# Kernel tuning notes

Measured on AMD Instinct MI355X. Metric: run time of the kernel, lower is better.

The kernel has to match this reference:

```python
import jax, jax.numpy as jnp
import numpy as np

D_MODEL = 512
NUM_HEADS = 8
D_K = D_MODEL // NUM_HEADS
D_FF = 4 * D_MODEL
EPS = 1e-5


def _pos_encoding(seq_len, d_model, dtype=jnp.float32):
    pos = jnp.arange(seq_len, dtype=jnp.float32)[:, None]              # [S,1]
    div = jnp.exp(jnp.arange(0, d_model, 2, dtype=jnp.float32) * (-np.log(10000.0) / d_model))  # [D/2]
    ang = pos * div                                                      # [S,D/2]
    pe = jnp.stack([jnp.sin(ang), jnp.cos(ang)], axis=-1).reshape(seq_len, d_model)
    return pe.astype(dtype)


def _layernorm(x, g, b):
    mu = jnp.mean(x, axis=-1, keepdims=True)
    var = jnp.mean(jnp.square(x - mu), axis=-1, keepdims=True)
    return (x - mu) * jax.lax.rsqrt(var + EPS) * g + b


def setup_inputs() -> dict:
    key = jax.random.key(0)
    ks = jax.random.split(key, 12)
    B, S, D = 4, 2048, D_MODEL
    s = 1.0 / np.sqrt(D)
    inp = {
        "x": jax.random.normal(ks[0], (B, S, D), jnp.float32),
        "Wq": jax.random.normal(ks[1], (D, D), jnp.float32) * s,
        "bq": jnp.zeros((D,), jnp.float32),
        "Wk": jax.random.normal(ks[2], (D, D), jnp.float32) * s,
        "bk": jnp.zeros((D,), jnp.float32),
        "Wv": jax.random.normal(ks[3], (D, D), jnp.float32) * s,
        "bv": jnp.zeros((D,), jnp.float32),
        "Wo": jax.random.normal(ks[4], (D, D), jnp.float32) * s,
        "bo": jnp.zeros((D,), jnp.float32),
        "g1": jnp.ones((D,), jnp.float32),
        "b1": jnp.zeros((D,), jnp.float32),
        "W_ff1": jax.random.normal(ks[5], (D, D_FF), jnp.float32) * s,
        "b_ff1": jnp.zeros((D_FF,), jnp.float32),
        "W_ff2": jax.random.normal(ks[6], (D_FF, D), jnp.float32) * (1.0 / np.sqrt(D_FF)),
        "b_ff2": jnp.zeros((D,), jnp.float32),
        "g2": jnp.ones((D,), jnp.float32),
        "b2": jnp.zeros((D,), jnp.float32),
    }
    return inp


def reference(x, Wq, bq, Wk, bk, Wv, bv, Wo, bo, g1, b1, W_ff1, b_ff1, W_ff2, b_ff2, g2, b2):
    B, S, D = x.shape
    H, dk = NUM_HEADS, D_K
    # positional encoding (deterministic buffer)
    x = x + _pos_encoding(S, D, x.dtype)[None]
    # projections -> [B,H,S,dk]
    q = (x @ Wq + bq).reshape(B, S, H, dk).transpose(0, 2, 1, 3)
    k = (x @ Wk + bk).reshape(B, S, H, dk).transpose(0, 2, 1, 3)
    v = (x @ Wv + bv).reshape(B, S, H, dk).transpose(0, 2, 1, 3)
    # naive attention: materialized [B,H,S,S] scores (as in original)
    scores = jnp.einsum('bhqd,bhkd->bhqk', q, k) / np.sqrt(dk)
    attn = jax.nn.softmax(scores, axis=-1)
    ctx = jnp.einsum('bhqk,bhkd->bhqd', attn, v)
    ctx = ctx.transpose(0, 2, 1, 3).reshape(B, S, D)
    attn_out = ctx @ Wo + bo
    # residual + LN + FFN + residual + LN
    h = _layernorm(x + attn_out, g1, b1)
    ff = jax.nn.relu(h @ W_ff1 + b_ff1) @ W_ff2 + b_ff2
    return _layernorm(h + ff, g2, b2)
```

## Files before the change

kernel.cpp:

```cpp
#include <hip/hip_runtime.h>

typedef unsigned short u16;
typedef unsigned int u32;
typedef __attribute__((ext_vector_type(8))) short s16x8;
typedef __attribute__((ext_vector_type(2))) float f32x2;
typedef __attribute__((ext_vector_type(4))) float f32x4;
typedef __attribute__((ext_vector_type(16))) float f32x16;
typedef __attribute__((ext_vector_type(2))) u32 u32x2;
typedef __attribute__((ext_vector_type(4))) u32 u32x4;

#define MB (1ull << 20)
#define K1SCALE 0.18033688f

__device__ __forceinline__ u16 f2bf(float f) {
  u32 u = __float_as_uint(f);
  u32 r = (u + 0x7fffu + ((u >> 16) & 1u)) >> 16;
  return (u16)r;
}

__device__ __forceinline__ float bf2f(u16 x) { return __uint_as_float(((u32)x) << 16); }

__device__ __forceinline__ u32 cvtpk(float lo, float hi) {
  u32 r;
  asm("v_cvt_pk_bf16_f32 %0, %1, %2" : "=v"(r) : "v"(lo), "v"(hi));
  return r;
}

__device__ __forceinline__ float max3f(float a, float b, float c) {
  float d;
  asm("v_max3_f32 %0, %1, %2, %3" : "=v"(d) : "v"(a), "v"(b), "v"(c));
  return d;
}

__device__ __forceinline__ f32x2 pk_mul(f32x2 a, f32x2 b) {
  f32x2 d;
  asm("v_pk_mul_f32 %0, %1, %2" : "=v"(d) : "v"(a), "v"(b));
  return d;
}
__device__ __forceinline__ f32x2 pk_add(f32x2 a, f32x2 b) {
  f32x2 d;
  asm("v_pk_add_f32 %0, %1, %2" : "=v"(d) : "v"(a), "v"(b));
  return d;
}

__device__ __forceinline__ void gload16(const u16* g, u16* l) {
  __builtin_amdgcn_global_load_lds((const __attribute__((address_space(1))) void*)g,
                                   (__attribute__((address_space(3))) void*)l, 16, 0, 0);
}

__global__ __launch_bounds__(256) void k_posenc(const float* __restrict__ x,
                                                float* __restrict__ xf, u16* __restrict__ xb) {
  int idx = blockIdx.x * 256 + threadIdx.x;
  int i2 = idx & 255;
  int srow = (idx >> 8) & 2047;
  float div = __expf((float)i2 * -0.03597789207803196f);
  float ang = (float)srow * div;
  f32x2 xv = *(const f32x2*)&x[(size_t)idx * 2];
  float v0 = xv[0] + __sinf(ang);
  float v1 = xv[1] + __cosf(ang);
  *(f32x2*)&xf[(size_t)idx * 2] = (f32x2){v0, v1};
  *(u32*)&xb[(size_t)idx * 2] = cvtpk(v0, v1);
}

__global__ __launch_bounds__(256) void k_wprep(const float* __restrict__ Wq, const float* __restrict__ Wk,
                                               const float* __restrict__ Wv, const float* __restrict__ Wo,
                                               const float* __restrict__ Wff1, const float* __restrict__ Wff2,
                                               const float* __restrict__ bq, const float* __restrict__ bk,
                                               const float* __restrict__ bv,
                                               u16* __restrict__ WqkvT, u16* __restrict__ WoT,
                                               u16* __restrict__ Wff1T, u16* __restrict__ Wff2T,
                                               float* __restrict__ bqkv) {
  __shared__ float tile[32][33];
  int id = blockIdx.x;
  if (id >= 3072) {
    int j = (id - 3072) * 256 + threadIdx.x;
    float v = (j < 512) ? bq[j] * K1SCALE : ((j < 1024) ? bk[j - 512] : bv[j - 1024]);
    bqkv[j] = v;
    return;
  }
  const float* W;
  u16* Wt;
  int K, N, k0, n0;
  float sc = 1.0f;
  if (id < 1024) {
    int mi = id >> 8, t = id & 255;
    K = 512; N = 512;
    k0 = (t & 15) * 32;
    n0 = (t >> 4) * 32;
    if (mi == 0) { W = Wq; Wt = WqkvT; sc = K1SCALE; }
    else if (mi == 1) { W = Wk; Wt = WqkvT + 512 * 512; }
    else if (mi == 2) { W = Wv; Wt = WqkvT + 2 * 512 * 512; }
    else { W = Wo; Wt = WoT; }
  } else if (id < 2048) {
    int t = id - 1024;
    K = 512; N = 2048;
    k0 = (t & 15) * 32;
    n0 = (t >> 4) * 32;
    W = Wff1; Wt = Wff1T;
  } else {
    int t = id - 2048;
    K = 2048; N = 512;
    k0 = (t >> 4) * 32;
    n0 = (t & 15) * 32;
    W = Wff2; Wt = Wff2T;
  }
  int tx = threadIdx.x & 31, ty = threadIdx.x >> 5;
  #pragma unroll
  for (int i = 0; i < 32; i += 8)
    tile[ty + i][tx] = W[(size_t)(k0 + ty + i) * N + n0 + tx];
  __syncthreads();
  #pragma unroll
  for (int i = 0; i < 32; i += 8)
    Wt[(size_t)(n0 + ty + i) * K + k0 + tx] = f2bf(tile[tx][ty + i] * sc);
}

template <int BN, bool RELU, bool WF32, bool WBF16>
__global__ __launch_bounds__(256) void k_gemm(const u16* __restrict__ A, const u16* __restrict__ Bt,
                                              const float* __restrict__ bias,
                                              float* __restrict__ Cf, u16* __restrict__ Cb,
                                              int N, int K) {
  constexpr int NACC = BN / 32;
  __shared__ u16 lA[128 * 64];
  __shared__ u16 lB[BN * 64];
  int t = threadIdx.x;
  int lane = t & 63;
  int w = t >> 6;
  int wm = w >> 1, wn = w & 1;
  int g = lane >> 4, c = lane & 15;
  size_t tm = (size_t)blockIdx.x * 128;
  size_t tn = (size_t)blockIdx.y * BN;

  f32x4 acc[4][NACC];
  #pragma unroll
  for (int i = 0; i < 4; i++)
    #pragma unroll
    for (int j = 0; j < NACC; j++) acc[i][j] = (f32x4){0.f, 0.f, 0.f, 0.f};

  for (int k0 = 0; k0 < K; k0 += 64) {
    __syncthreads();
    #pragma unroll
    for (int i = 0; i < 4; i++) {
      int ch = t + i * 256;
      int row = ch >> 3;
      int koff = ((ch ^ row) & 7) << 3;
      gload16(A + (tm + row) * K + k0 + koff, lA + ch * 8);
    }
    #pragma unroll
    for (int i = 0; i < BN / 32; i++) {
      int ch = t + i * 256;
      int row = ch >> 3;
      int koff = ((ch ^ row) & 7) << 3;
      gload16(Bt + (tn + row) * K + k0 + koff, lB + ch * 8);
    }
    __syncthreads();
    #pragma unroll
    for (int kh = 0; kh < 2; kh++) {
      int sl = ((g + 4 * kh) ^ (c & 7)) << 3;
      s16x8 af[4], bf[NACC];
      #pragma unroll
      for (int i = 0; i < 4; i++)
        af[i] = *(const s16x8*)&lA[(wm * 64 + i * 16 + c) * 64 + sl];
      #pragma unroll
      for (int j = 0; j < NACC; j++)
        bf[j] = *(const s16x8*)&lB[(wn * (BN / 2) + j * 16 + c) * 64 + sl];
      #pragma unroll
      for (int i = 0; i < 4; i++)
        #pragma unroll
        for (int j = 0; j < NACC; j++)
          acc[i][j] = __builtin_amdgcn_mfma_f32_16x16x32_bf16(af[i], bf[j], acc[i][j], 0, 0, 0);
    }
  }
  #pragma unroll
  for (int j = 0; j < NACC; j++) {
    size_t col = tn + wn * (BN / 2) + j * 16 + c;
    float bv = bias[col];
    #pragma unroll
    for (int i = 0; i < 4; i++) {
      size_t row0 = tm + wm * 64 + i * 16 + g * 4;
      #pragma unroll
      for (int r = 0; r < 4; r++) {
        float v = acc[i][j][r] + bv;
        if (RELU) v = fmaxf(v, 0.0f);
        if (WF32) Cf[(row0 + r) * N + col] = v;
        if (WBF16) Cb[(row0 + r) * N + col] = f2bf(v);
      }
    }
  }
}

__global__ __launch_bounds__(256) void k_vt(const u16* __restrict__ qkv, u16* __restrict__ vT) {
  __shared__ u16 tile[32][33];
  int bh = blockIdx.z;
  int b = bh >> 3, h = bh & 7;
  int s0 = blockIdx.x * 32, d0 = blockIdx.y * 32;
  int tx = threadIdx.x & 31, ty = threadIdx.x >> 5;
  #pragma unroll
  for (int i = 0; i < 32; i += 8)
    tile[ty + i][tx] = qkv[(size_t)(b * 2048 + s0 + ty + i) * 1536 + 1024 + h * 64 + d0 + tx];
  __syncthreads();
  #pragma unroll
  for (int i = 0; i < 32; i += 8)
    vT[(size_t)(bh * 64 + d0 + ty + i) * 2048 + s0 + tx] = tile[tx][ty + i];
}

union F16U {
  f32x16 v;
  f32x2 p[8];
};

__global__ __launch_bounds__(512, 4) void k_attn(const u16* __restrict__ qkv,
                                                 const u16* __restrict__ vT,
                                                 u16* __restrict__ ctx) {
  __shared__ u16 lds[8][4096];
  int t = threadIdx.x;
  int w = t >> 6, lane = t & 63;
  int qg = w >> 1, kh = w & 1;
  int ql = lane & 31, hi = lane >> 5;
  int bh = blockIdx.y;
  int b = bh >> 3, h = bh & 7;
  int q0 = blockIdx.x * 128 + qg * 32;
  int r7 = ql & 7;

  int sh = t >> 8;
  int th = t & 255;
  const u16* kbaseg = qkv + (size_t)(b * 2048 + sh * 1024) * 1536 + 512 + h * 64;
  const u16* vbaseg = vT + (size_t)(bh * 64) * 2048 + sh * 1024;

  auto stage = [&](int buf, int step) {
    int t0 = step * 64;
    #pragma unroll
    for (int i = 0; i < 2; i++) {
      int ch = th + i * 256;
      int row = ch >> 3;
      int off = ((ch ^ row) & 7) << 3;
      gload16(kbaseg + (size_t)(t0 + row) * 1536 + off, &lds[(sh * 2 + buf) * 2][ch * 8]);
      gload16(vbaseg + (size_t)row * 2048 + t0 + off, &lds[(sh * 2 + buf) * 2 + 1][ch * 8]);
    }
  };

  const u16* qbase = qkv + (size_t)(b * 2048 + q0 + ql) * 1536 + h * 64 + hi * 8;
  s16x8 qf[4];
  #pragma unroll
  for (int ks = 0; ks < 4; ks++) qf[ks] = *(const s16x8*)(qbase + ks * 16);

  float m = -1e30f, l = 0.f;
  F16U O0, O1;
  #pragma unroll
  for (int i = 0; i < 16; i++) { O0.v[i] = 0.f; O1.v[i] = 0.f; }

  stage(0, 0);

  for (int step = 0; step < 16; ++step) {
    int buf = step & 1;
    asm volatile("s_waitcnt vmcnt(0)" ::: "memory");
    __builtin_amdgcn_s_barrier();
    __builtin_amdgcn_sched_barrier(0);
    if (step < 15) stage(buf ^ 1, step + 1);

    const u16* lK = lds[(kh * 2 + buf) * 2];
    const u16* lV = lds[(kh * 2 + buf) * 2 + 1];

    F16U S0, S1;
    #pragma unroll
    for (int i = 0; i < 16; i++) { S0.v[i] = 0.f; S1.v[i] = 0.f; }
    #pragma unroll
    for (int ks = 0; ks < 4; ks++) {
      int so = ((ks * 2 + hi) ^ r7) << 3;
      s16x8 kf0 = *(const s16x8*)&lK[ql * 64 + so];
      s16x8 kf1 = *(const s16x8*)&lK[(32 + ql) * 64 + so];
      S0.v = __builtin_amdgcn_mfma_f32_32x32x16_bf16(kf0, qf[ks], S0.v, 0, 0, 0);
      S1.v = __builtin_amdgcn_mfma_f32_32x32x16_bf16(kf1, qf[ks], S1.v, 0, 0, 0);
    }

    float a0 = max3f(S0.v[0], S0.v[1], S0.v[2]);
    float a1 = max3f(S0.v[3], S0.v[4], S0.v[5]);
    float a2 = max3f(S0.v[6], S0.v[7], S0.v[8]);
    float a3 = max3f(S0.v[9], S0.v[10], S0.v[11]);
    float a4 = max3f(S0.v[12], S0.v[13], S0.v[14]);
    float a5 = max3f(S0.v[15], S1.v[0], S1.v[1]);
    float a6 = max3f(S1.v[2], S1.v[3], S1.v[4]);
    float a7 = max3f(S1.v[5], S1.v[6], S1.v[7]);
    float a8 = max3f(S1.v[8], S1.v[9], S1.v[10]);
    float a9 = max3f(S1.v[11], S1.v[12], S1.v[13]);
    float a10 = fmaxf(S1.v[14], S1.v[15]);
    float b0 = max3f(a0, a1, a2);
    float b1 = max3f(a3, a4, a5);
    float b2 = max3f(a6, a7, a8);
    float b3 = max3f(a9, a10, b0);
    float rm = max3f(b1, b2, b3);
    rm = fmaxf(rm, __shfl_xor(rm, 32, 64));

    if (!__all(rm <= m + 8.0f)) {
      float mn = fmaxf(m, rm);
      float al = __builtin_amdgcn_exp2f(m - mn);
      m = mn;
      f32x2 alp = {al, al};
      #pragma unroll
      for (int i = 0; i < 8; i++) {
        O0.p[i] = pk_mul(O0.p[i], alp);
        O1.p[i] = pk_mul(O1.p[i], alp);
      }
      l *= al;
    }

    f32x2 nmp = {-m, -m};
    #pragma unroll
    for (int i = 0; i < 8; i++) {
      S0.p[i] = pk_add(S0.p[i], nmp);
      S1.p[i] = pk_add(S1.p[i], nmp);
    }
    #pragma unroll
    for (int i = 0; i < 16; i++) {
      S0.v[i] = __builtin_amdgcn_exp2f(S0.v[i]);
      S1.v[i] = __builtin_amdgcn_exp2f(S1.v[i]);
    }
    f32x2 c0 = pk_add(S0.p[0], S0.p[1]);
    f32x2 c1 = pk_add(S0.p[2], S0.p[3]);
    f32x2 c2 = pk_add(S0.p[4], S0.p[5]);
    f32x2 c3 = pk_add(S0.p[6], S0.p[7]);
    f32x2 d0 = pk_add(S1.p[0], S1.p[1]);
    f32x2 d1 = pk_add(S1.p[2], S1.p[3]);
    f32x2 d2 = pk_add(S1.p[4], S1.p[5]);
    f32x2 d3 = pk_add(S1.p[6], S1.p[7]);
    c0 = pk_add(c0, c1);
    c2 = pk_add(c2, c3);
    d0 = pk_add(d0, d1);
    d2 = pk_add(d2, d3);
    c0 = pk_add(c0, c2);
    d0 = pk_add(d0, d2);
    c0 = pk_add(c0, d0);
    float pssum = c0[0] + c0[1];
    pssum += __shfl_xor(pssum, 32, 64);
    l += pssum;

    auto pv = [&](const f32x16& sv, int kb) {
      u32 a0w = cvtpk(sv[0], sv[1]), a1w = cvtpk(sv[2], sv[3]);
      u32 a2w = cvtpk(sv[4], sv[5]), a3w = cvtpk(sv[6], sv[7]);
      u32 b0w = cvtpk(sv[8], sv[9]), b1w = cvtpk(sv[10], sv[11]);
      u32 b2w = cvtpk(sv[12], sv[13]), b3w = cvtpk(sv[14], sv[15]);
      asm("v_permlane32_swap_b32 %0, %1" : "+v"(a0w), "+v"(a2w));
      asm("v_permlane32_swap_b32 %0, %1" : "+v"(a1w), "+v"(a3w));
      asm("v_permlane32_swap_b32 %0, %1" : "+v"(b0w), "+v"(b2w));
      asm("v_permlane32_swap_b32 %0, %1" : "+v"(b1w), "+v"(b3w));
      u32x4 w0v = {a0w, a1w, a2w, a3w};
      u32x4 w1v = {b0w, b1w, b2w, b3w};
      s16x8 pf0 = __builtin_bit_cast(s16x8, w0v);
      s16x8 pf1 = __builtin_bit_cast(s16x8, w1v);
      int base0 = ((kb * 4 + hi) ^ r7) << 3;
      int base1 = ((kb * 4 + 2 + hi) ^ r7) << 3;
      s16x8 vf00 = *(const s16x8*)&lV[ql * 64 + base0];
      s16x8 vf01 = *(const s16x8*)&lV[ql * 64 + base1];
      s16x8 vf10 = *(const s16x8*)&lV[(32 + ql) * 64 + base0];
      s16x8 vf11 = *(const s16x8*)&lV[(32 + ql) * 64 + base1];
      O0.v = __builtin_amdgcn_mfma_f32_32x32x16_bf16(vf00, pf0, O0.v, 0, 0, 0);
      O0.v = __builtin_amdgcn_mfma_f32_32x32x16_bf16(vf01, pf1, O0.v, 0, 0, 0);
      O1.v = __builtin_amdgcn_mfma_f32_32x32x16_bf16(vf10, pf0, O1.v, 0, 0, 0);
      O1.v = __builtin_amdgcn_mfma_f32_32x32x16_bf16(vf11, pf1, O1.v, 0, 0, 0);
    };
    pv(S0.v, 0);
    pv(S1.v, 1);
  }

  asm volatile("s_waitcnt lgkmcnt(0)" ::: "memory");
  __builtin_amdgcn_s_barrier();
  float* mrg = (float*)&lds[0][0];
  float* p = mrg + (size_t)(qg * 64 + lane) * 36;
  if (kh == 1) {
    p[0] = m;
    p[1] = l;
    #pragma unroll
    for (int i = 0; i < 16; i++) {
      p[2 + i] = O0.v[i];
      p[18 + i] = O1.v[i];
    }
  }
  asm volatile("s_waitcnt lgkmcnt(0)" ::: "memory");
  __builtin_amdgcn_s_barrier();
  if (kh == 0) {
    float m1 = p[0], l1 = p[1];
    float M = fmaxf(m, m1);
    float sc0 = __builtin_amdgcn_exp2f(m - M);
    float sc1 = __builtin_amdgcn_exp2f(m1 - M);
    float L = sc0 * l + sc1 * l1;
    float inv = 1.0f / L;
    sc0 *= inv;
    sc1 *= inv;
    size_t obase = (size_t)(b * 2048 + q0 + ql) * 512 + h * 64;
    #pragma unroll
    for (int k = 0; k < 4; k++) {
      float v0 = O0.v[4 * k] * sc0 + p[2 + 4 * k] * sc1;
      float v1 = O0.v[4 * k + 1] * sc0 + p[2 + 4 * k + 1] * sc1;
      float v2 = O0.v[4 * k + 2] * sc0 + p[2 + 4 * k + 2] * sc1;
      float v3 = O0.v[4 * k + 3] * sc0 + p[2 + 4 * k + 3] * sc1;
      u32x2 p0 = {cvtpk(v0, v1), cvtpk(v2, v3)};
      *(u32x2*)&ctx[obase + 8 * k + 4 * hi] = p0;
      float u0 = O1.v[4 * k] * sc0 + p[18 + 4 * k] * sc1;
      float u1 = O1.v[4 * k + 1] * sc0 + p[18 + 4 * k + 1] * sc1;
      float u2 = O1.v[4 * k + 2] * sc0 + p[18 + 4 * k + 2] * sc1;
      float u3 = O1.v[4 * k + 3] * sc0 + p[18 + 4 * k + 3] * sc1;
      u32x2 p1 = {cvtpk(u0, u1), cvtpk(u2, u3)};
      *(u32x2*)&ctx[obase + 32 + 8 * k + 4 * hi] = p1;
    }
  }
}

template <bool WB>
__global__ __launch_bounds__(256) void k_addln(const float* __restrict__ A, const float* __restrict__ Bv,
                                               const float* __restrict__ G, const float* __restrict__ Bb,
                                               float* __restrict__ Of, u16* __restrict__ Ob) {
  int row = blockIdx.x;
  int t = threadIdx.x;
  size_t base = (size_t)row * 512 + 2 * t;
  f32x2 av = *(const f32x2*)&A[base];
  f32x2 bv = *(const f32x2*)&Bv[base];
  float x0 = av[0] + bv[0];
  float x1 = av[1] + bv[1];
  float s = x0 + x1;
  #pragma unroll
  for (int d = 1; d < 64; d <<= 1) s += __shfl_xor(s, d, 64);
  __shared__ float red[8];
  int w = t >> 6, lane = t & 63;
  if (lane == 0) red[w] = s;
  __syncthreads();
  float mu = (red[0] + red[1] + red[2] + red[3]) * (1.0f / 512.0f);
  float d0 = x0 - mu, d1 = x1 - mu;
  float vs = d0 * d0 + d1 * d1;
  #pragma unroll
  for (int d = 1; d < 64; d <<= 1) vs += __shfl_xor(vs, d, 64);
  if (lane == 0) red[4 + w] = vs;
  __syncthreads();
  float var = (red[4] + red[5] + red[6] + red[7]) * (1.0f / 512.0f);
  float rs = rsqrtf(var + 1e-5f);
  f32x2 gg = *(const f32x2*)&G[2 * t];
  f32x2 bb = *(const f32x2*)&Bb[2 * t];
  float o0 = d0 * rs * gg[0] + bb[0];
  float o1 = d1 * rs * gg[1] + bb[1];
  *(f32x2*)&Of[base] = (f32x2){o0, o1};
  if (WB) *(u32*)&Ob[base] = cvtpk(o0, o1);
}

extern "C" void kernel_launch(void* const* d_in, const int* in_sizes, int n_in,
                              void* d_out, int out_size, void* d_ws, size_t ws_size,
                              hipStream_t stream) {
  const float* x = (const float*)d_in[0];
  const float* Wq = (const float*)d_in[1];
  const float* bq = (const float*)d_in[2];
  const float* Wk = (const float*)d_in[3];
  const float* bk = (const float*)d_in[4];
  const float* Wv = (const float*)d_in[5];
  const float* bv = (const float*)d_in[6];
  const float* Wo = (const float*)d_in[7];
  const float* bo = (const float*)d_in[8];
  const float* g1 = (const float*)d_in[9];
  const float* b1 = (const float*)d_in[10];
  const float* Wff1 = (const float*)d_in[11];
  const float* bff1 = (const float*)d_in[12];
  const float* Wff2 = (const float*)d_in[13];
  const float* bff2 = (const float*)d_in[14];
  const float* g2 = (const float*)d_in[15];
  const float* b2 = (const float*)d_in[16];

  char* ws = (char*)d_ws;
  float* xpe_f = (float*)(ws + 0);
  u16* xpe_b = (u16*)(ws + 16 * MB);
  u16* qkv = (u16*)(ws + 24 * MB);
  u16* vT = (u16*)(ws + 48 * MB);
  u16* ctx = (u16*)(ws + 56 * MB);
  float* ao = (float*)(ws + 64 * MB);
  float* hf = (float*)(ws + 80 * MB);
  u16* hb = (u16*)(ws + 96 * MB);
  u16* ff1 = (u16*)(ws + 24 * MB);
  u16* WqkvT = (u16*)(ws + 104 * MB);
  u16* WoT = (u16*)(ws + 106 * MB);
  u16* Wff1T = (u16*)(ws + 107 * MB);
  u16* Wff2T = (u16*)(ws + 109 * MB);
  float* bqkv = (float*)(ws + 111 * MB);
  (void)in_sizes; (void)n_in; (void)out_size; (void)ws_size;

  k_posenc<<<8192, 256, 0, stream>>>(x, xpe_f, xpe_b);
  k_wprep<<<3078, 256, 0, stream>>>(Wq, Wk, Wv, Wo, Wff1, Wff2, bq, bk, bv,
                                    WqkvT, WoT, Wff1T, Wff2T, bqkv);

  k_gemm<128, false, false, true><<<dim3(64, 12), 256, 0, stream>>>(xpe_b, WqkvT, bqkv, nullptr, qkv, 1536, 512);
  k_vt<<<dim3(64, 2, 32), 256, 0, stream>>>(qkv, vT);
  k_attn<<<dim3(16, 32), 512, 0, stream>>>(qkv, vT, ctx);
  k_gemm<64, false, true, false><<<dim3(64, 8), 256, 0, stream>>>(ctx, WoT, bo, ao, nullptr, 512, 512);
  k_addln<true><<<8192, 256, 0, stream>>>(xpe_f, ao, g1, b1, hf, hb);
  k_gemm<128, true, false, true><<<dim3(64, 16), 256, 0, stream>>>(hb, Wff1T, bff1, nullptr, ff1, 2048, 512);
  k_gemm<64, false, true, false><<<dim3(64, 8), 256, 0, stream>>>(ff1, Wff2T, bff2, ao, nullptr, 512, 2048);
  k_addln<false><<<8192, 256, 0, stream>>>(hf, ao, g2, b2, (float*)d_out, nullptr);
}
```

Measured before the change: 189.9 us.

## Add triple-buffered 256x128 GEMM and fuse V transpose into QKV epilogue

Adds a new GEMM kernel with 256x128 tiles, 512 threads, triple-buffered LDS with XOR swizzle, split-phase MFMA, and s_setprio, so global loads overlap compute. It is used for the QKV and FFN1 projections. The QKV epilogue writes the V columns directly in transposed layout, which removes the separate k_vt transpose kernel and its extra pass over V. The kernel uses much more LDS (about 144KB), which limits occupancy, and the grids shrink to 384 and 512 blocks, which may underfill the CUs.

Result: faster. 185.5 us (-2.3%).

```diff
diff --git a/kernel.cpp b/kernel.cpp
--- a/kernel.cpp
+++ b/kernel.cpp
@@ -114,6 +114,139 @@
     Wt[(size_t)(n0 + ty + i) * K + k0 + tx] = f2bf(tile[tx][ty + i] * sc);
 }
 
+template <int NK, bool RELU, bool QKV>
+__global__ __launch_bounds__(512, 2) void k_gemm3(const u16* __restrict__ A, const u16* __restrict__ Bt,
+                                                  const float* __restrict__ bias, u16* __restrict__ Cb,
+                                                  u16* __restrict__ vTout, int N) {
+  constexpr int K = NK * 64;
+  __shared__ u16 lA[3][256 * 64];
+  __shared__ u16 lB[3][128 * 64];
+  int t = threadIdx.x;
+  int lane = t & 63;
+  int w = t >> 6;
+  int wr = w >> 1, wc = w & 1;
+  int g = lane >> 4, c = lane & 15;
+  size_t tm = (size_t)blockIdx.x * 256;
+  size_t tn = (size_t)blockIdx.y * 128;
+
+  auto stg = [&](int buf, int kt, int half) {
+    int k0 = kt * 64;
+    #pragma unroll
+    for (int i = 0; i < 2; i++) {
+      int ch = t + (half * 2 + i) * 512;
+      int row = ch >> 3;
+      int koff = ((ch ^ row) & 7) << 3;
+      gload16(A + (tm + row) * K + k0 + koff, &lA[buf][ch * 8]);
+    }
+    int ch = t + half * 512;
+    int row = ch >> 3;
+    int koff = ((ch ^ row) & 7) << 3;
+    gload16(Bt + (tn + row) * K + k0 + koff, &lB[buf][ch * 8]);
+  };
+
+  f32x4 acc[4][4];
+  #pragma unroll
+  for (int i = 0; i < 4; i++)
+    #pragma unroll
+    for (int j = 0; j < 4; j++) acc[i][j] = (f32x4){0.f, 0.f, 0.f, 0.f};
+
+  stg(0, 0, 0); stg(0, 0, 1);
+  stg(1, 1, 0); stg(1, 1, 1);
+  asm volatile("s_waitcnt vmcnt(6)" ::: "memory");
+  __builtin_amdgcn_s_barrier();
+  __builtin_amdgcn_sched_barrier(0);
+
+  #pragma unroll
+  for (int kt = 0; kt < NK; kt++) {
+    const int buf = kt % 3;
+    const int nb = (kt + 2) % 3;
+    s16x8 bfr[4][2], afr[2][2];
+    #pragma unroll
+    for (int nr = 0; nr < 4; nr++)
+      #pragma unroll
+      for (int ks = 0; ks < 2; ks++)
+        bfr[nr][ks] = *(const s16x8*)&lB[buf][(wc * 64 + nr * 16 + c) * 64 + (((g + 4 * ks) ^ (c & 7)) << 3)];
+    #pragma unroll
+    for (int mr = 0; mr < 2; mr++)
+      #pragma unroll
+      for (int ks = 0; ks < 2; ks++)
+        afr[mr][ks] = *(const s16x8*)&lA[buf][(wr * 64 + mr * 16 + c) * 64 + (((g + 4 * ks) ^ (c & 7)) << 3)];
+    if (kt + 2 < NK) stg(nb, kt + 2, 0);
+    __builtin_amdgcn_s_barrier();
+    __builtin_amdgcn_sched_barrier(0);
+    __builtin_amdgcn_s_setprio(1);
+    #pragma unroll
+    for (int mr = 0; mr < 2; mr++)
+      #pragma unroll
+      for (int nr = 0; nr < 4; nr++)
+        #pragma unroll
+        for (int ks = 0; ks < 2; ks++)
+          acc[mr][nr] = __builtin_amdgcn_mfma_f32_16x16x32_bf16(afr[mr][ks], bfr[nr][ks], acc[mr][nr], 0, 0, 0);
+    __builtin_amdgcn_s_setprio(0);
+    __builtin_amdgcn_s_barrier();
+    __builtin_amdgcn_sched_barrier(0);
+    #pragma unroll
+    for (int mr = 0; mr < 2; mr++)
+      #pragma unroll
+      for (int ks = 0; ks < 2; ks++)
+        afr[mr][ks] = *(const s16x8*)&lA[buf][(wr * 64 + (mr + 2) * 16 + c) * 64 + (((g + 4 * ks) ^ (c & 7)) << 3)];
+    if (kt + 2 < NK) stg(nb, kt + 2, 1);
+    __builtin_amdgcn_s_barrier();
+    __builtin_amdgcn_sched_barrier(0);
+    __builtin_amdgcn_s_setprio(1);
+    #pragma unroll
+    for (int mr = 0; mr < 2; mr++)
+      #pragma unroll
+      for (int nr = 0; nr < 4; nr++)
+        #pragma unroll
+        for (int ks = 0; ks < 2; ks++)
+          acc[mr + 2][nr] = __builtin_amdgcn_mfma_f32_16x16x32_bf16(afr[mr][ks], bfr[nr][ks], acc[mr + 2][nr], 0, 0, 0);
+    __builtin_amdgcn_s_setprio(0);
+    if (kt < NK - 1) {
+      if (kt + 2 < NK)
+        asm volatile("s_waitcnt vmcnt(6)" ::: "memory");
+      else
+        asm volatile("s_waitcnt vmcnt(0)" ::: "memory");
+      __builtin_amdgcn_s_barrier();
+      __builtin_amdgcn_sched_barrier(0);
+    }
+  }
+
+  if (QKV && tn >= 1024) {
+    #pragma unroll
+    for (int mr = 0; mr < 4; mr++) {
+      int row0 = (int)tm + wr * 64 + mr * 16 + g * 4;
+      int b = row0 >> 11, s0 = row0 & 2047;
+      #pragma unroll
+      for (int nr = 0; nr < 4; nr++) {
+        int colr = (int)(tn - 1024) + wc * 64 + nr * 16 + c;
+        int h = colr >> 6, d = colr & 63;
+        float bv = bias[1024 + colr];
+        u32 w0 = cvtpk(acc[mr][nr][0] + bv, acc[mr][nr][1] + bv);
+        u32 w1 = cvtpk(acc[mr][nr][2] + bv, acc[mr][nr][3] + bv);
+        u32x2 pp = {w0, w1};
+        *(u32x2*)&vTout[((size_t)((b << 3) + h) * 64 + d) * 2048 + s0] = pp;
+      }
+    }
+  } else {
+    #pragma unroll
+    for (int nr = 0; nr < 4; nr++) {
+      size_t col = tn + wc * 64 + nr * 16 + c;
+      float bv = bias[col];
+      #pragma unroll
+      for (int mr = 0; mr < 4; mr++) {
+        size_t row0 = tm + wr * 64 + mr * 16 + g * 4;
+        #pragma unroll
+        for (int r = 0; r < 4; r++) {
+          float v = acc[mr][nr][r] + bv;
+          if (RELU) v = fmaxf(v, 0.0f);
+          Cb[(row0 + r) * N + col] = f2bf(v);
+        }
+      }
+    }
+  }
+}
+
 template <int BN, bool RELU, bool WF32, bool WBF16>
 __global__ __launch_bounds__(256) void k_gemm(const u16* __restrict__ A, const u16* __restrict__ Bt,
                                               const float* __restrict__ bias,
@@ -186,21 +319,6 @@
       }
     }
   }
-}
-
-__global__ __launch_bounds__(256) void k_vt(const u16* __restrict__ qkv, u16* __restrict__ vT) {
-  __shared__ u16 tile[32][33];
-  int bh = blockIdx.z;
-  int b = bh >> 3, h = bh & 7;
-  int s0 = blockIdx.x * 32, d0 = blockIdx.y * 32;
-  int tx = threadIdx.x & 31, ty = threadIdx.x >> 5;
-  #pragma unroll
-  for (int i = 0; i < 32; i += 8)
-    tile[ty + i][tx] = qkv[(size_t)(b * 2048 + s0 + ty + i) * 1536 + 1024 + h * 64 + d0 + tx];
-  __syncthreads();
-  #pragma unroll
-  for (int i = 0; i < 32; i += 8)
-    vT[(size_t)(bh * 64 + d0 + ty + i) * 2048 + s0 + tx] = tile[tx][ty + i];
 }
 
 union F16U {
@@ -481,12 +599,11 @@
   k_wprep<<<3078, 256, 0, stream>>>(Wq, Wk, Wv, Wo, Wff1, Wff2, bq, bk, bv,
                                     WqkvT, WoT, Wff1T, Wff2T, bqkv);
 
-  k_gemm<128, false, false, true><<<dim3(64, 12), 256, 0, stream>>>(xpe_b, WqkvT, bqkv, nullptr, qkv, 1536, 512);
-  k_vt<<<dim3(64, 2, 32), 256, 0, stream>>>(qkv, vT);
+  k_gemm3<8, false, true><<<dim3(32, 12), 512, 0, stream>>>(xpe_b, WqkvT, bqkv, qkv, vT, 1536);
   k_attn<<<dim3(16, 32), 512, 0, stream>>>(qkv, vT, ctx);
   k_gemm<64, false, true, false><<<dim3(64, 8), 256, 0, stream>>>(ctx, WoT, bo, ao, nullptr, 512, 512);
   k_addln<true><<<8192, 256, 0, stream>>>(xpe_f, ao, g1, b1, hf, hb);
-  k_gemm<128, true, false, true><<<dim3(64, 16), 256, 0, stream>>>(hb, Wff1T, bff1, nullptr, ff1, 2048, 512);
+  k_gemm3<8, true, false><<<dim3(32, 16), 512, 0, stream>>>(hb, Wff1T, bff1, ff1, nullptr, 2048);
   k_gemm<64, false, true, false><<<dim3(64, 8), 256, 0, stream>>>(ff1, Wff2T, bff2, ao, nullptr, 512, 2048);
   k_addln<false><<<8192, 256, 0, stream>>>(hf, ao, g2, b2, (float*)d_out, nullptr);
 }
```
